# Performance work log

Measured on AMD Instinct MI355X. Metric: run time of the kernel, lower is better.

The kernel has to match this reference:

```python
import jax, jax.numpy as jnp
import numpy as np

EMBED_DIM = 1024
NUM_HEADS = 16
HEAD_DIM = EMBED_DIM // NUM_HEADS


def setup_inputs() -> dict:
    key = jax.random.key(0)
    ks = jax.random.split(key, 7)
    B, N, C = 2, 2048, EMBED_DIM
    s = 1.0 / np.sqrt(C)
    return {
        "x": jax.random.normal(ks[0], (B, N, C), dtype=jnp.float32),
        "phase_signal": jax.random.uniform(ks[1], (B,), dtype=jnp.float32),
        "qkv_w": jax.random.normal(ks[2], (3 * C, C), dtype=jnp.float32) * s,
        "qkv_b": jnp.zeros((3 * C,), dtype=jnp.float32),
        "proj_w": jax.random.normal(ks[3], (C, C), dtype=jnp.float32) * s,
        "proj_b": jnp.zeros((C,), dtype=jnp.float32),
        "phase_weight": jnp.ones((NUM_HEADS,), dtype=jnp.float32),
    }


def reference(x, phase_signal, qkv_w, qkv_b, proj_w, proj_b, phase_weight):
    B, N, C = x.shape
    H, D = NUM_HEADS, HEAD_DIM
    # qkv projection: [B,N,3C] -> [3,B,H,N,D]
    qkv = (x @ qkv_w.T + qkv_b).reshape(B, N, 3, H, D)
    qkv = jnp.transpose(qkv, (2, 0, 3, 1, 4))
    q, k, v = qkv[0], qkv[1], qkv[2]
    attn = jnp.einsum("bhnd,bhmd->bhnm", q, k) * (D ** -0.5)
    # per-(batch, head) phase modulation applied before softmax
    phase_mod = phase_weight[None, :, None, None] * phase_signal[:, None, None, None]
    attn = attn * (1.0 + 0.2 * phase_mod)
    attn = jax.nn.softmax(attn, axis=-1)  # dropout is identity in eval mode
    out = jnp.einsum("bhnm,bhmd->bhnd", attn, v)
    out = jnp.transpose(out, (0, 2, 1, 3)).reshape(B, N, C)
    return out @ proj_w.T + proj_b
```

## Files before the change

### kernel.cpp

```cpp
#include <hip/hip_runtime.h>
#include <stdint.h>

#define NUM_H 16
#define HD    64
#define CDIM  1024
#define NSEQ  2048
#define NBATCH 2
#define LOG2E 1.4426950408889634f

typedef __attribute__((ext_vector_type(8))) short short8;
typedef __attribute__((ext_vector_type(4))) float f32x4;
typedef __attribute__((ext_vector_type(16))) float f32x16;
typedef __attribute__((ext_vector_type(4))) unsigned short ushort4v;
typedef __attribute__((ext_vector_type(4))) float float4v;
typedef __attribute__((ext_vector_type(2))) unsigned int u32x2;

__device__ __forceinline__ unsigned short f2bf(float f) {
    unsigned int u = __builtin_bit_cast(unsigned int, f);
    unsigned int r = u + 0x7fffu + ((u >> 16) & 1u);
    return (unsigned short)(r >> 16);
}

__device__ __forceinline__ float bf2f(unsigned short u) {
    return __builtin_bit_cast(float, (unsigned int)u << 16);
}

__device__ __forceinline__ unsigned int cvtpk(float a, float b) {
    unsigned int r;
    asm("v_cvt_pk_bf16_f32 %0, %1, %2" : "=v"(r) : "v"(a), "v"(b));
    return r;
}

__device__ __forceinline__ void plswap(unsigned int &a, unsigned int &b) {
    asm("v_permlane32_swap_b32 %0, %1" : "+v"(a), "+v"(b));
}

__device__ __forceinline__ void gload_lds16(const void* g, const void* l) {
    __builtin_amdgcn_global_load_lds(
        (const __attribute__((address_space(1))) unsigned int*)(unsigned long long)(uintptr_t)g,
        (__attribute__((address_space(3))) unsigned int*)(unsigned int)(uintptr_t)l,
        16, 0, 0);
}

__global__ void cvt_all_kernel(const float* __restrict__ x,
                               const float* __restrict__ w1,
                               const float* __restrict__ wp,
                               unsigned short* __restrict__ xo,
                               unsigned short* __restrict__ w1o,
                               unsigned short* __restrict__ wpo) {
    int i = blockIdx.x * blockDim.x + threadIdx.x;
    const float* in; unsigned short* out;
    if (i < 1048576)      { in = x;  out = xo; }
    else if (i < 1835008) { in = w1; out = w1o; i -= 1048576; }
    else                  { in = wp; out = wpo; i -= 1835008; }
    float4v v = *(const float4v*)(in + (size_t)i * 4);
    ushort4v o;
    o[0] = f2bf(v[0]); o[1] = f2bf(v[1]); o[2] = f2bf(v[2]); o[3] = f2bf(v[3]);
    *(ushort4v*)(out + (size_t)i * 4) = o;
}

__global__ __launch_bounds__(512, 2) void gemm_qkv(
    const unsigned short* __restrict__ A,
    const unsigned short* __restrict__ Bw,
    const float* __restrict__ bias,
    const float* __restrict__ ps,
    const float* __restrict__ pw,
    unsigned short* __restrict__ qb,
    unsigned short* __restrict__ kfrag,
    unsigned short* __restrict__ vfrag)
{
    __shared__ unsigned short lds[2][2][2][128][64];

    const int tid = threadIdx.x;
    const int wid = tid >> 6;
    const int lane = tid & 63;
    const int l15 = lane & 15, l4 = lane >> 4;
    const int wave_m = wid >> 2, wave_n = wid & 3;

    const int bm = blockIdx.x;
    const int bn = blockIdx.y;

    f32x4 acc[8][4];
    const f32x4 zero4 = {0.f, 0.f, 0.f, 0.f};
#pragma unroll
    for (int m = 0; m < 8; ++m)
#pragma unroll
        for (int n = 0; n < 4; ++n) acc[m][n] = zero4;

    const int jr = lane >> 3;
    const int jc = ((lane & 7) ^ jr) << 4;
    const char* aB = (const char*)A  + (size_t)(bm * 256) * 2048;
    const char* bB = (const char*)Bw + (size_t)(bn * 256) * 2048;

    auto stageH = [&](int t, int which) {
        const int buf = t & 1;
        const int op = which >> 1, hf = which & 1;
        const char* src = (op == 0) ? aB : bB;
        const int rowb = hf * 128 + wid * 16;
        const size_t k0b = (size_t)t * 128;
        char* dst = (char*)&lds[buf][op][hf][wid * 16][0];
#pragma unroll
        for (int i = 0; i < 2; ++i)
            gload_lds16(src + (size_t)(rowb + i * 8 + jr) * 2048 + k0b + jc,
                        dst + i * 1024);
    };

    const int swz = (l15 & 7) << 4;
    auto rdA = [&](int buf, int mq, int mp, int kk) -> short8 {
        return *(const short8*)((const char*)&lds[buf][0][wave_m][mq * 64 + mp * 16 + l15][0]
                                + ((kk * 64 + l4 * 16) ^ swz));
    };
    auto rdB = [&](int buf, int nq, int np, int kk) -> short8 {
        const int br = wave_n * 64 + nq * 32 + np * 16 + l15;
        return *(const short8*)((const char*)&lds[buf][1][br >> 7][br & 127][0]
                                + ((kk * 64 + l4 * 16) ^ swz));
    };

    stageH(0, 0); stageH(0, 1); stageH(0, 2); stageH(0, 3);
    stageH(1, 2); stageH(1, 3); stageH(1, 0); stageH(1, 1);
    asm volatile("s_waitcnt vmcnt(8)" ::: "memory");
    __builtin_amdgcn_s_barrier();

    for (int t = 0; t < 16; ++t) {
        const int buf = t & 1;
        short8 af[4][2], bf[2][2][2];

#pragma unroll
        for (int mp = 0; mp < 4; ++mp) {
            af[mp][0] = rdA(buf, 0, mp, 0); af[mp][1] = rdA(buf, 0, mp, 1);
        }
#pragma unroll
        for (int np = 0; np < 2; ++np) {
            bf[0][np][0] = rdB(buf, 0, np, 0); bf[0][np][1] = rdB(buf, 0, np, 1);
        }
        __builtin_amdgcn_s_barrier();
        __builtin_amdgcn_s_setprio(1);
#pragma unroll
        for (int mp = 0; mp < 4; ++mp)
#pragma unroll
            for (int np = 0; np < 2; ++np)
#pragma unroll
                for (int kk = 0; kk < 2; ++kk)
                    acc[mp][np] = __builtin_amdgcn_mfma_f32_16x16x32_bf16(
                        af[mp][kk], bf[0][np][kk], acc[mp][np], 0, 0, 0);
        __builtin_amdgcn_s_setprio(0);
        __builtin_amdgcn_s_barrier();

#pragma unroll
        for (int np = 0; np < 2; ++np) {
            bf[1][np][0] = rdB(buf, 1, np, 0); bf[1][np][1] = rdB(buf, 1, np, 1);
        }
        if (t < 14) stageH(t + 2, 2);
        __builtin_amdgcn_s_barrier();
        __builtin_amdgcn_s_setprio(1);
#pragma unroll
        for (int mp = 0; mp < 4; ++mp)
#pragma unroll
            for (int np = 0; np < 2; ++np)
#pragma unroll
                for (int kk = 0; kk < 2; ++kk)
                    acc[mp][2 + np] = __builtin_amdgcn_mfma_f32_16x16x32_bf16(
                        af[mp][kk], bf[1][np][kk], acc[mp][2 + np], 0, 0, 0);
        __builtin_amdgcn_s_setprio(0);
        __builtin_amdgcn_s_barrier();

#pragma unroll
        for (int mp = 0; mp < 4; ++mp) {
            af[mp][0] = rdA(buf, 1, mp, 0); af[mp][1] = rdA(buf, 1, mp, 1);
        }
        if (t < 14) stageH(t + 2, 3);
        __builtin_amdgcn_s_barrier();
        __builtin_amdgcn_s_setprio(1);
#pragma unroll
        for (int mp = 0; mp < 4; ++mp)
#pragma unroll
            for (int np = 0; np < 2; ++np)
#pragma unroll
                for (int kk = 0; kk < 2; ++kk)
                    acc[4 + mp][np] = __builtin_amdgcn_mfma_f32_16x16x32_bf16(
                        af[mp][kk], bf[0][np][kk], acc[4 + mp][np], 0, 0, 0);
        __builtin_amdgcn_s_setprio(0);
        __builtin_amdgcn_s_barrier();

        if (t < 14) { stageH(t + 2, 0); stageH(t + 2, 1); }
        __builtin_amdgcn_s_barrier();
        __builtin_amdgcn_s_setprio(1);
#pragma unroll
        for (int mp = 0; mp < 4; ++mp)
#pragma unroll
            for (int np = 0; np < 2; ++np)
#pragma unroll
                for (int kk = 0; kk < 2; ++kk)
                    acc[4 + mp][2 + np] = __builtin_amdgcn_mfma_f32_16x16x32_bf16(
                        af[mp][kk], bf[1][np][kk], acc[4 + mp][2 + np], 0, 0, 0);
        __builtin_amdgcn_s_setprio(0);
        if (t < 14)       { asm volatile("s_waitcnt vmcnt(8)" ::: "memory"); }
        else if (t == 14) { asm volatile("s_waitcnt vmcnt(0)" ::: "memory"); }
        __builtin_amdgcn_s_barrier();
    }

    const int col_base = bn * 256 + wave_n * 64;
    const int t3b = bn >> 2;
    const int bb = bm >> 3;
    const int nn0 = (bm & 7) * 256;
    char* tbc = (char*)&lds[0][0][0][0][0];

    __syncthreads();

    if (t3b == 0) {
#pragma unroll
        for (int n = 0; n < 4; ++n) {
            const int d = n * 16 + l15;
            const float bv = bias[col_base + n * 16 + l15];
#pragma unroll
            for (int m = 0; m < 8; ++m) {
#pragma unroll
                for (int r = 0; r < 4; ++r) {
                    const int tt = wave_m * 128 + m * 16 + l4 * 4 + r;
                    *(unsigned short*)(tbc + wave_n * 32768 + tt * 128 +
                                       ((d * 2) ^ ((tt & 7) << 4))) = f2bf(acc[m][n][r] + bv);
                }
            }
        }
        __syncthreads();
#pragma unroll
        for (int i = 0; i < 16; ++i) {
            const int hq = i >> 2, sub = i & 3;
            const int tt = sub * 64 + (tid >> 3);
            const int chunk = tid & 7;
            const short8 v = *(const short8*)(tbc + hq * 32768 + tt * 128 +
                                              ((chunk * 16) ^ ((tt & 7) << 4)));
            *(short8*)(qb + ((size_t)(bb * 16 + bn * 4 + hq) * 2048 + nn0 + tt) * 64 + chunk * 8) = v;
        }
    } else if (t3b == 1) {
        const float ps0 = ps[0], ps1 = ps[1];
        const int hh = (bn - 4) * 4 + wave_n;
        const float kf = 0.125f * LOG2E *
                         (1.f + 0.2f * pw[hh] * ((bb == 0) ? ps0 : ps1));
#pragma unroll
        for (int n = 0; n < 4; ++n) {
            const int hi_ = l15 >> 3, e = l15 & 7;
            const float bv = bias[col_base + n * 16 + l15];
#pragma unroll
            for (int m = 0; m < 8; ++m) {
#pragma unroll
                for (int r = 0; r < 4; ++r) {
                    const int tt = wave_m * 128 + m * 16 + l4 * 4 + r;
                    const int ti = tt >> 6, u = tt & 63;
                    const int s_ = u >> 5, l31_ = u & 31;
                    *(unsigned short*)(tbc + (((wave_n * 4 + ti) * 8 + s_ * 4 + n) << 10) +
                                       ((hi_ * 32 + l31_) << 4) + e * 2) =
                        f2bf((acc[m][n][r] + bv) * kf);
                }
            }
        }
        __syncthreads();
#pragma unroll
        for (int i = 0; i < 16; ++i) {
            const int hq = i >> 2, ti = i & 3;
            const short8 v = *(const short8*)(tbc + i * 8192 + tid * 16);
            *(short8*)(kfrag + ((size_t)(bb * 16 + (bn - 4) * 4 + hq) * 32 +
                                ((bm & 7) * 4 + ti)) * 4096 + tid * 8) = v;
        }
    } else {
#pragma unroll
        for (int n = 0; n < 4; ++n) {
            const int d = n * 16 + l15;
            const int dt_ = n >> 1, l31_ = d & 31;
            const float bv = bias[col_base + n * 16 + l15];
#pragma unroll
            for (int m = 0; m < 8; ++m) {
#pragma unroll
                for (int r = 0; r < 4; ++r) {
                    const int tt = wave_m * 128 + m * 16 + l4 * 4 + r;
                    const int ti = tt >> 6, u = tt & 63;
                    const int ks = u >> 4, hi_ = (u >> 3) & 1, e = u & 7;
                    *(unsigned short*)(tbc + (((wave_n * 4 + ti) * 8 + dt_ * 4 + ks) << 10) +
                                       ((hi_ * 32 + l31_) << 4) + e * 2) =
                        f2bf(acc[m][n][r] + bv);
                }
            }
        }
        __syncthreads();
#pragma unroll
        for (int i = 0; i < 16; ++i) {
            const int hq = i >> 2, ti = i & 3;
            const short8 v = *(const short8*)(tbc + i * 8192 + tid * 16);
            *(short8*)(vfrag + ((size_t)(bb * 16 + (bn - 8) * 4 + hq) * 32 +
                                ((bm & 7) * 4 + ti)) * 4096 + tid * 8) = v;
        }
    }
}

__global__ __launch_bounds__(256, 2) void gemm_proj(
    const unsigned short* __restrict__ A,
    const unsigned short* __restrict__ Bw,
    const float* __restrict__ bias,
    float* __restrict__ out)
{
    __shared__ unsigned short As[2][128 * 64];
    __shared__ unsigned short Bs[2][128 * 64];
    const int tid = threadIdx.x;
    const int wid = tid >> 6;
    const int lane = tid & 63;
    const int l15 = lane & 15, l4 = lane >> 4;
    const int bm = blockIdx.x, bn = blockIdx.y;
    const int wr = wid >> 1, wc = wid & 1;

    f32x4 acc[4][4];
    const f32x4 zero4 = {0.f, 0.f, 0.f, 0.f};
#pragma unroll
    for (int m = 0; m < 4; ++m)
#pragma unroll
        for (int n = 0; n < 4; ++n) acc[m][n] = zero4;

    const int jr = lane >> 3;
    const int jc = ((lane & 7) ^ jr) << 4;
    const char* aB = (const char*)A  + (size_t)(bm * 128) * 2048;
    const char* bB = (const char*)Bw + (size_t)(bn * 128) * 2048;

    auto stage = [&](int buf, int k0) {
#pragma unroll
        for (int i = 0; i < 4; ++i) {
            const int rowb = wid * 32 + i * 8;
            gload_lds16(aB + (size_t)(rowb + jr) * 2048 + k0 * 2 + jc,
                        (const char*)&As[buf][0] + rowb * 128);
            gload_lds16(bB + (size_t)(rowb + jr) * 2048 + k0 * 2 + jc,
                        (const char*)&Bs[buf][0] + rowb * 128);
        }
    };

    const int swz = (l15 & 7) << 4;

    stage(0, 0);
    for (int it = 0; it < 16; ++it) {
        const int buf = it & 1;
        __syncthreads();
        if (it < 15) stage(buf ^ 1, (it + 1) * 64);
#pragma unroll
        for (int kk = 0; kk < 2; ++kk) {
            short8 a[4], b[4];
#pragma unroll
            for (int m = 0; m < 4; ++m)
                a[m] = *(const short8*)((const char*)&As[buf][0] +
                        (wr * 64 + m * 16 + l15) * 128 + ((kk * 64 + l4 * 16) ^ swz));
#pragma unroll
            for (int n = 0; n < 4; ++n)
                b[n] = *(const short8*)((const char*)&Bs[buf][0] +
                        (wc * 64 + n * 16 + l15) * 128 + ((kk * 64 + l4 * 16) ^ swz));
            __builtin_amdgcn_s_setprio(1);
#pragma unroll
            for (int m = 0; m < 4; ++m)
#pragma unroll
                for (int n = 0; n < 4; ++n)
                    acc[m][n] = __builtin_amdgcn_mfma_f32_16x16x32_bf16(a[m], b[n], acc[m][n], 0, 0, 0);
            __builtin_amdgcn_s_setprio(0);
        }
    }

    const int row_base = bm * 128 + wr * 64;
    const int col_base = bn * 128 + wc * 64;
#pragma unroll
    for (int n = 0; n < 4; ++n) {
        const int col = col_base + n * 16 + l15;
        const float bv = bias[col];
#pragma unroll
        for (int m = 0; m < 4; ++m) {
#pragma unroll
            for (int r = 0; r < 4; ++r) {
                const int row = row_base + m * 16 + l4 * 4 + r;
                out[(size_t)row * 1024 + col] = acc[m][n][r] + bv;
            }
        }
    }
}

__global__ __launch_bounds__(256, 4) void attn_kernel(
    const unsigned short* __restrict__ qb,
    const unsigned short* __restrict__ kfrag,
    const unsigned short* __restrict__ vfrag,
    unsigned short* __restrict__ o0,
    unsigned short* __restrict__ o1,
    float* __restrict__ lrb)
{
    __shared__ unsigned short KVs[2][2][4096];

    const int tid = threadIdx.x;
    const int w = tid >> 6;
    const int l = tid & 63;
    const int l31 = l & 31;
    const int hi = l >> 5;

    const int bid = blockIdx.y * 32 + blockIdx.x;
    const int wg = (bid & 7) * 128 + (bid >> 3);
    const int bh = wg >> 5;
    const int r5 = wg & 31;
    const int qt = r5 >> 1, kvh = r5 & 1;
    const int b = bh >> 4, h = bh & 15;
    const int q0 = qt * 128 + w * 32;

    const char* qg = (const char*)(qb + (size_t)bh * 2048 * 64);
    const unsigned short* kg = kfrag + ((size_t)bh * 32 + kvh * 16) * 4096;
    const unsigned short* vg = vfrag + ((size_t)bh * 32 + kvh * 16) * 4096;

    short8 qf[4];
#pragma unroll
    for (int t = 0; t < 4; ++t)
        qf[t] = *(const short8*)(qg + (size_t)(q0 + l31) * 128 + t * 32 + hi * 16);

    f32x16 oacc[2];
#pragma unroll
    for (int dt = 0; dt < 2; ++dt)
#pragma unroll
        for (int r = 0; r < 16; ++r) oacc[dt][r] = 0.f;
    float lr = 0.f;

    auto stage = [&](int buf, int T) {
#pragma unroll
        for (int i = 0; i < 2; ++i) {
            const int c = w * 2 + i;
            gload_lds16(kg + (size_t)T * 4096 + c * 512 + l * 8, &KVs[buf][0][c * 512]);
            gload_lds16(vg + (size_t)T * 4096 + c * 512 + l * 8, &KVs[buf][1][c * 512]);
        }
    };

    stage(0, 0);
    __syncthreads();

    for (int it = 0; it < 16; ++it) {
        const int buf = it & 1;
        if (it < 15) stage(buf ^ 1, it + 1);

        const unsigned short* Kb = &KVs[buf][0][0];
        const unsigned short* Vb = &KVs[buf][1][0];

        f32x16 sa[2];
        __builtin_amdgcn_s_setprio(1);
#pragma unroll
        for (int s = 0; s < 2; ++s) {
#pragma unroll
            for (int r = 0; r < 16; ++r) sa[s][r] = 0.f;
#pragma unroll
            for (int t = 0; t < 4; ++t) {
                const short8 kf = *(const short8*)(Kb + (s * 4 + t) * 512 + l * 8);
                sa[s] = __builtin_amdgcn_mfma_f32_32x32x16_bf16(kf, qf[t], sa[s], 0, 0, 0);
            }
        }
        __builtin_amdgcn_s_setprio(0);

#pragma unroll
        for (int s = 0; s < 2; ++s)
#pragma unroll
            for (int r = 0; r < 16; ++r)
                sa[s][r] = __builtin_amdgcn_exp2f(sa[s][r] - 20.0f);

        float ts[16];
#pragma unroll
        for (int r = 0; r < 16; ++r) ts[r] = sa[0][r] + sa[1][r];
#pragma unroll
        for (int d = 8; d >= 1; d >>= 1)
#pragma unroll
            for (int r = 0; r < 8; ++r)
                if (r < d) ts[r] += ts[r + d];
        lr += ts[0] + __shfl_xor(ts[0], 32);

#pragma unroll
        for (int s = 0; s < 2; ++s) {
            unsigned int wv[8];
#pragma unroll
            for (int g = 0; g < 8; ++g)
                wv[g] = cvtpk(sa[s][g * 2], sa[s][g * 2 + 1]);
            plswap(wv[0], wv[2]); plswap(wv[1], wv[3]);
            plswap(wv[4], wv[6]); plswap(wv[5], wv[7]);
            union { unsigned int u[4]; short8 s8; } f0, f1;
            f0.u[0] = wv[0]; f0.u[1] = wv[1]; f0.u[2] = wv[2]; f0.u[3] = wv[3];
            f1.u[0] = wv[4]; f1.u[1] = wv[5]; f1.u[2] = wv[6]; f1.u[3] = wv[7];
            __builtin_amdgcn_s_setprio(1);
#pragma unroll
            for (int dt = 0; dt < 2; ++dt) {
                const short8 v0 = *(const short8*)(Vb + (dt * 4 + s * 2 + 0) * 512 + l * 8);
                oacc[dt] = __builtin_amdgcn_mfma_f32_32x32x16_bf16(v0, f0.s8, oacc[dt], 0, 0, 0);
                const short8 v1 = *(const short8*)(Vb + (dt * 4 + s * 2 + 1) * 512 + l * 8);
                oacc[dt] = __builtin_amdgcn_mfma_f32_32x32x16_bf16(v1, f1.s8, oacc[dt], 0, 0, 0);
            }
            __builtin_amdgcn_s_setprio(0);
        }
        __syncthreads();
    }

    const float inv = 1.0f / lr;
    unsigned short* ob = kvh ? o1 : o0;
    char* outp = (char*)ob + ((size_t)(b * 2048 + q0 + l31) * 1024 + h * 64) * 2;
#pragma unroll
    for (int dt = 0; dt < 2; ++dt)
#pragma unroll
        for (int rg = 0; rg < 4; ++rg) {
            u32x2 pkd;
            pkd[0] = cvtpk(oacc[dt][rg * 4 + 0] * inv, oacc[dt][rg * 4 + 1] * inv);
            pkd[1] = cvtpk(oacc[dt][rg * 4 + 2] * inv, oacc[dt][rg * 4 + 3] * inv);
            *(u32x2*)(outp + (size_t)(dt * 32 + rg * 8 + hi * 4) * 2) = pkd;
        }
    if (hi == 0)
        lrb[(kvh << 16) + (bh << 11) + q0 + l31] = lr;
}

__global__ void combine_kernel(unsigned short* __restrict__ o0,
                               const unsigned short* __restrict__ o1,
                               const float* __restrict__ lrb) {
    const int idx = blockIdx.x * blockDim.x + threadIdx.x;
    const size_t e0 = (size_t)idx * 8;
    const int row = (int)(e0 >> 10);
    const int col = (int)(e0 & 1023);
    const int b = row >> 11, q = row & 2047, h = col >> 6;
    const int bhq = ((b * 16 + h) << 11) + q;
    const float l0 = lrb[bhq], l1 = lrb[65536 + bhq];
    const float w0 = l0 / (l0 + l1);
    const float w1 = 1.0f - w0;
    short8 v0 = *(short8*)(o0 + e0);
    const short8 v1 = *(const short8*)(o1 + e0);
    short8 o;
#pragma unroll
    for (int j = 0; j < 8; ++j)
        o[j] = (short)f2bf(bf2f((unsigned short)v0[j]) * w0 +
                           bf2f((unsigned short)v1[j]) * w1);
    *(short8*)(o0 + e0) = o;
}

extern "C" void kernel_launch(void* const* d_in, const int* in_sizes, int n_in,
                              void* d_out, int out_size, void* d_ws, size_t ws_size,
                              hipStream_t stream) {
    const float* x      = (const float*)d_in[0];
    const float* ps     = (const float*)d_in[1];
    const float* qkv_w  = (const float*)d_in[2];
    const float* qkv_b  = (const float*)d_in[3];
    const float* proj_w = (const float*)d_in[4];
    const float* proj_b = (const float*)d_in[5];
    const float* pw     = (const float*)d_in[6];
    float* out = (float*)d_out;
    char* ws = (char*)d_ws;

    unsigned short* x_bf    = (unsigned short*)(ws);
    unsigned short* w1_bf   = (unsigned short*)(ws + (8u  << 20));
    unsigned short* wp_bf   = (unsigned short*)(ws + (14u << 20));
    unsigned short* qb      = (unsigned short*)(ws + (16u << 20));
    unsigned short* kfrag   = (unsigned short*)(ws + (24u << 20));
    unsigned short* vfrag   = (unsigned short*)(ws + (32u << 20));
    unsigned short* o1      = (unsigned short*)(ws + (40u << 20));
    unsigned short* o0      = x_bf;
    float*          lrb     = (float*)w1_bf;
    unsigned short* attn_bf = o0;

    cvt_all_kernel<<<8192, 256, 0, stream>>>(x, qkv_w, proj_w, x_bf, w1_bf, wp_bf);
    gemm_qkv<<<dim3(16, 12), 512, 0, stream>>>(x_bf, w1_bf, qkv_b, ps, pw, qb, kfrag, vfrag);
    attn_kernel<<<dim3(32, 32), 256, 0, stream>>>(qb, kfrag, vfrag, o0, o1, lrb);
    combine_kernel<<<2048, 256, 0, stream>>>(o0, o1, lrb);
    gemm_proj<<<dim3(32, 8), 256, 0, stream>>>(attn_bf, wp_bf, proj_b, out);
}
```

Before: 113.0 us.

## Retile QKV GEMM to 256x192 with 12 waves; MFMA row-sums and deeper attention pipeline

The QKV GEMM moves from 256x256 tiles with 8 waves to 256x192 tiles with 12 waves, giving a 16x16 grid of blocks and a unified epilogue that handles Q/K/V per 64-column region. The attention kernel computes the softmax denominator with an MFMA against a ones vector instead of shuffle reductions. It also prefetches two K/V tiles ahead with explicit waitcnt-based synchronisation. These changes aim to improve CU occupancy and balance, remove ALU reduction work, and overlap loads better, at the cost of more LDS use and extra MFMA work.

```diff
diff --git a/kernel.cpp b/kernel.cpp
--- a/kernel.cpp
+++ b/kernel.cpp
@@ -59,7 +59,7 @@
     *(ushort4v*)(out + (size_t)i * 4) = o;
 }
 
-__global__ __launch_bounds__(512, 2) void gemm_qkv(
+__global__ __launch_bounds__(768, 3) void gemm_qkv(
     const unsigned short* __restrict__ A,
     const unsigned short* __restrict__ Bw,
     const float* __restrict__ bias,
@@ -69,225 +69,165 @@
     unsigned short* __restrict__ kfrag,
     unsigned short* __restrict__ vfrag)
 {
-    __shared__ unsigned short lds[2][2][2][128][64];
+    __shared__ unsigned short smem[57344];
+    unsigned short* As = smem;
+    unsigned short* Bs = smem + 32768;
 
     const int tid = threadIdx.x;
     const int wid = tid >> 6;
     const int lane = tid & 63;
     const int l15 = lane & 15, l4 = lane >> 4;
-    const int wave_m = wid >> 2, wave_n = wid & 3;
+    const int wave_n = wid >> 2;
+    const int wave_m = wid & 3;
 
     const int bm = blockIdx.x;
     const int bn = blockIdx.y;
 
-    f32x4 acc[8][4];
+    f32x4 acc[4][4];
     const f32x4 zero4 = {0.f, 0.f, 0.f, 0.f};
 #pragma unroll
-    for (int m = 0; m < 8; ++m)
+    for (int m = 0; m < 4; ++m)
 #pragma unroll
         for (int n = 0; n < 4; ++n) acc[m][n] = zero4;
 
     const int jr = lane >> 3;
     const int jc = ((lane & 7) ^ jr) << 4;
     const char* aB = (const char*)A  + (size_t)(bm * 256) * 2048;
-    const char* bB = (const char*)Bw + (size_t)(bn * 256) * 2048;
-
-    auto stageH = [&](int t, int which) {
+    const char* bB = (const char*)Bw + (size_t)(bn * 192) * 2048;
+
+    auto stage = [&](int t) {
         const int buf = t & 1;
-        const int op = which >> 1, hf = which & 1;
-        const char* src = (op == 0) ? aB : bB;
-        const int rowb = hf * 128 + wid * 16;
-        const size_t k0b = (size_t)t * 128;
-        char* dst = (char*)&lds[buf][op][hf][wid * 16][0];
-#pragma unroll
-        for (int i = 0; i < 2; ++i)
-            gload_lds16(src + (size_t)(rowb + i * 8 + jr) * 2048 + k0b + jc,
-                        dst + i * 1024);
+        const size_t kb = (size_t)t * 128;
+        for (int s = wid; s < 32; s += 12)
+            gload_lds16(aB + (size_t)(s * 8 + jr) * 2048 + kb + jc,
+                        (char*)(As + buf * 16384) + s * 1024);
+        for (int s = wid; s < 24; s += 12)
+            gload_lds16(bB + (size_t)(s * 8 + jr) * 2048 + kb + jc,
+                        (char*)(Bs + buf * 12288) + s * 1024);
     };
 
     const int swz = (l15 & 7) << 4;
-    auto rdA = [&](int buf, int mq, int mp, int kk) -> short8 {
-        return *(const short8*)((const char*)&lds[buf][0][wave_m][mq * 64 + mp * 16 + l15][0]
-                                + ((kk * 64 + l4 * 16) ^ swz));
-    };
-    auto rdB = [&](int buf, int nq, int np, int kk) -> short8 {
-        const int br = wave_n * 64 + nq * 32 + np * 16 + l15;
-        return *(const short8*)((const char*)&lds[buf][1][br >> 7][br & 127][0]
-                                + ((kk * 64 + l4 * 16) ^ swz));
-    };
-
-    stageH(0, 0); stageH(0, 1); stageH(0, 2); stageH(0, 3);
-    stageH(1, 2); stageH(1, 3); stageH(1, 0); stageH(1, 1);
-    asm volatile("s_waitcnt vmcnt(8)" ::: "memory");
+
+    stage(0); stage(1);
+    asm volatile("s_waitcnt vmcnt(4)" ::: "memory");
     __builtin_amdgcn_s_barrier();
 
     for (int t = 0; t < 16; ++t) {
         const int buf = t & 1;
-        short8 af[4][2], bf[2][2][2];
-
-#pragma unroll
-        for (int mp = 0; mp < 4; ++mp) {
-            af[mp][0] = rdA(buf, 0, mp, 0); af[mp][1] = rdA(buf, 0, mp, 1);
-        }
-#pragma unroll
-        for (int np = 0; np < 2; ++np) {
-            bf[0][np][0] = rdB(buf, 0, np, 0); bf[0][np][1] = rdB(buf, 0, np, 1);
-        }
+        __builtin_amdgcn_s_setprio(1);
+#pragma unroll
+        for (int kk = 0; kk < 2; ++kk) {
+            short8 a[4], b[4];
+#pragma unroll
+            for (int m = 0; m < 4; ++m)
+                a[m] = *(const short8*)((const char*)(As + buf * 16384) +
+                        (wave_m * 64 + m * 16 + l15) * 128 + ((kk * 64 + l4 * 16) ^ swz));
+#pragma unroll
+            for (int n = 0; n < 4; ++n)
+                b[n] = *(const short8*)((const char*)(Bs + buf * 12288) +
+                        (wave_n * 64 + n * 16 + l15) * 128 + ((kk * 64 + l4 * 16) ^ swz));
+#pragma unroll
+            for (int m = 0; m < 4; ++m)
+#pragma unroll
+                for (int n = 0; n < 4; ++n)
+                    acc[m][n] = __builtin_amdgcn_mfma_f32_16x16x32_bf16(a[m], b[n], acc[m][n], 0, 0, 0);
+        }
+        __builtin_amdgcn_s_setprio(0);
+        asm volatile("s_waitcnt lgkmcnt(0)" ::: "memory");
         __builtin_amdgcn_s_barrier();
-        __builtin_amdgcn_s_setprio(1);
-#pragma unroll
-        for (int mp = 0; mp < 4; ++mp)
-#pragma unroll
-            for (int np = 0; np < 2; ++np)
-#pragma unroll
-                for (int kk = 0; kk < 2; ++kk)
-                    acc[mp][np] = __builtin_amdgcn_mfma_f32_16x16x32_bf16(
-                        af[mp][kk], bf[0][np][kk], acc[mp][np], 0, 0, 0);
-        __builtin_amdgcn_s_setprio(0);
-        __builtin_amdgcn_s_barrier();
-
-#pragma unroll
-        for (int np = 0; np < 2; ++np) {
-            bf[1][np][0] = rdB(buf, 1, np, 0); bf[1][np][1] = rdB(buf, 1, np, 1);
-        }
-        if (t < 14) stageH(t + 2, 2);
-        __builtin_amdgcn_s_barrier();
-        __builtin_amdgcn_s_setprio(1);
-#pragma unroll
-        for (int mp = 0; mp < 4; ++mp)
-#pragma unroll
-            for (int np = 0; np < 2; ++np)
-#pragma unroll
-                for (int kk = 0; kk < 2; ++kk)
-                    acc[mp][2 + np] = __builtin_amdgcn_mfma_f32_16x16x32_bf16(
-                        af[mp][kk], bf[1][np][kk], acc[mp][2 + np], 0, 0, 0);
-        __builtin_amdgcn_s_setprio(0);
-        __builtin_amdgcn_s_barrier();
-
-#pragma unroll
-        for (int mp = 0; mp < 4; ++mp) {
-            af[mp][0] = rdA(buf, 1, mp, 0); af[mp][1] = rdA(buf, 1, mp, 1);
-        }
-        if (t < 14) stageH(t + 2, 3);
-        __builtin_amdgcn_s_barrier();
-        __builtin_amdgcn_s_setprio(1);
-#pragma unroll
-        for (int mp = 0; mp < 4; ++mp)
-#pragma unroll
-            for (int np = 0; np < 2; ++np)
-#pragma unroll
-                for (int kk = 0; kk < 2; ++kk)
-                    acc[4 + mp][np] = __builtin_amdgcn_mfma_f32_16x16x32_bf16(
-                        af[mp][kk], bf[0][np][kk], acc[4 + mp][np], 0, 0, 0);
-        __builtin_amdgcn_s_setprio(0);
-        __builtin_amdgcn_s_barrier();
-
-        if (t < 14) { stageH(t + 2, 0); stageH(t + 2, 1); }
-        __builtin_amdgcn_s_barrier();
-        __builtin_amdgcn_s_setprio(1);
-#pragma unroll
-        for (int mp = 0; mp < 4; ++mp)
-#pragma unroll
-            for (int np = 0; np < 2; ++np)
-#pragma unroll
-                for (int kk = 0; kk < 2; ++kk)
-                    acc[4 + mp][2 + np] = __builtin_amdgcn_mfma_f32_16x16x32_bf16(
-                        af[mp][kk], bf[1][np][kk], acc[4 + mp][2 + np], 0, 0, 0);
-        __builtin_amdgcn_s_setprio(0);
-        if (t < 14)       { asm volatile("s_waitcnt vmcnt(8)" ::: "memory"); }
-        else if (t == 14) { asm volatile("s_waitcnt vmcnt(0)" ::: "memory"); }
+        if (t < 14) {
+            stage(t + 2);
+            asm volatile("s_waitcnt vmcnt(4)" ::: "memory");
+        } else if (t == 14) {
+            asm volatile("s_waitcnt vmcnt(0)" ::: "memory");
+        }
         __builtin_amdgcn_s_barrier();
     }
 
-    const int col_base = bn * 256 + wave_n * 64;
-    const int t3b = bn >> 2;
+    __syncthreads();
+    char* tbc = (char*)smem;
     const int bb = bm >> 3;
-    const int nn0 = (bm & 7) * 256;
-    char* tbc = (char*)&lds[0][0][0][0][0];
-
-    __syncthreads();
-
-    if (t3b == 0) {
+    const int cb = bn * 192 + wave_n * 64;
+    const int t3w = cb >> 10;
+    const int hh_w = (cb >> 6) & 15;
+    float kf = 1.f;
+    if (t3w == 1)
+        kf = 0.125f * LOG2E * (1.f + 0.2f * pw[hh_w] * ((bb == 0) ? ps[0] : ps[1]));
+
+    if (t3w == 0) {
 #pragma unroll
         for (int n = 0; n < 4; ++n) {
             const int d = n * 16 + l15;
-            const float bv = bias[col_base + n * 16 + l15];
-#pragma unroll
-            for (int m = 0; m < 8; ++m) {
+            const float bv = bias[cb + n * 16 + l15];
+#pragma unroll
+            for (int m = 0; m < 4; ++m)
 #pragma unroll
                 for (int r = 0; r < 4; ++r) {
-                    const int tt = wave_m * 128 + m * 16 + l4 * 4 + r;
+                    const int tt = wave_m * 64 + m * 16 + l4 * 4 + r;
                     *(unsigned short*)(tbc + wave_n * 32768 + tt * 128 +
                                        ((d * 2) ^ ((tt & 7) << 4))) = f2bf(acc[m][n][r] + bv);
                 }
-            }
-        }
-        __syncthreads();
-#pragma unroll
-        for (int i = 0; i < 16; ++i) {
-            const int hq = i >> 2, sub = i & 3;
-            const int tt = sub * 64 + (tid >> 3);
-            const int chunk = tid & 7;
-            const short8 v = *(const short8*)(tbc + hq * 32768 + tt * 128 +
-                                              ((chunk * 16) ^ ((tt & 7) << 4)));
-            *(short8*)(qb + ((size_t)(bb * 16 + bn * 4 + hq) * 2048 + nn0 + tt) * 64 + chunk * 8) = v;
-        }
-    } else if (t3b == 1) {
-        const float ps0 = ps[0], ps1 = ps[1];
-        const int hh = (bn - 4) * 4 + wave_n;
-        const float kf = 0.125f * LOG2E *
-                         (1.f + 0.2f * pw[hh] * ((bb == 0) ? ps0 : ps1));
+        }
+    } else if (t3w == 1) {
 #pragma unroll
         for (int n = 0; n < 4; ++n) {
             const int hi_ = l15 >> 3, e = l15 & 7;
-            const float bv = bias[col_base + n * 16 + l15];
-#pragma unroll
-            for (int m = 0; m < 8; ++m) {
+            const float bv = bias[cb + n * 16 + l15];
+#pragma unroll
+            for (int m = 0; m < 4; ++m)
 #pragma unroll
                 for (int r = 0; r < 4; ++r) {
-                    const int tt = wave_m * 128 + m * 16 + l4 * 4 + r;
-                    const int ti = tt >> 6, u = tt & 63;
+                    const int tt = wave_m * 64 + m * 16 + l4 * 4 + r;
+                    const int T_ = tt >> 6, u = tt & 63;
                     const int s_ = u >> 5, l31_ = u & 31;
-                    *(unsigned short*)(tbc + (((wave_n * 4 + ti) * 8 + s_ * 4 + n) << 10) +
+                    *(unsigned short*)(tbc + wave_n * 32768 + ((T_ * 8 + s_ * 4 + n) << 10) +
                                        ((hi_ * 32 + l31_) << 4) + e * 2) =
                         f2bf((acc[m][n][r] + bv) * kf);
                 }
-            }
-        }
-        __syncthreads();
-#pragma unroll
-        for (int i = 0; i < 16; ++i) {
-            const int hq = i >> 2, ti = i & 3;
-            const short8 v = *(const short8*)(tbc + i * 8192 + tid * 16);
-            *(short8*)(kfrag + ((size_t)(bb * 16 + (bn - 4) * 4 + hq) * 32 +
-                                ((bm & 7) * 4 + ti)) * 4096 + tid * 8) = v;
         }
     } else {
 #pragma unroll
         for (int n = 0; n < 4; ++n) {
-            const int d = n * 16 + l15;
-            const int dt_ = n >> 1, l31_ = d & 31;
-            const float bv = bias[col_base + n * 16 + l15];
-#pragma unroll
-            for (int m = 0; m < 8; ++m) {
+            const int dt_ = n >> 1;
+            const int l31v = (n & 1) * 16 + l15;
+            const float bv = bias[cb + n * 16 + l15];
+#pragma unroll
+            for (int m = 0; m < 4; ++m)
 #pragma unroll
                 for (int r = 0; r < 4; ++r) {
-                    const int tt = wave_m * 128 + m * 16 + l4 * 4 + r;
-                    const int ti = tt >> 6, u = tt & 63;
+                    const int tt = wave_m * 64 + m * 16 + l4 * 4 + r;
+                    const int T_ = tt >> 6, u = tt & 63;
                     const int ks = u >> 4, hi_ = (u >> 3) & 1, e = u & 7;
-                    *(unsigned short*)(tbc + (((wave_n * 4 + ti) * 8 + dt_ * 4 + ks) << 10) +
-                                       ((hi_ * 32 + l31_) << 4) + e * 2) =
+                    *(unsigned short*)(tbc + wave_n * 32768 + ((T_ * 8 + dt_ * 4 + ks) << 10) +
+                                       ((hi_ * 32 + l31v) << 4) + e * 2) =
                         f2bf(acc[m][n][r] + bv);
                 }
-            }
-        }
-        __syncthreads();
-#pragma unroll
-        for (int i = 0; i < 16; ++i) {
-            const int hq = i >> 2, ti = i & 3;
-            const short8 v = *(const short8*)(tbc + i * 8192 + tid * 16);
-            *(short8*)(vfrag + ((size_t)(bb * 16 + (bn - 8) * 4 + hq) * 32 +
-                                ((bm & 7) * 4 + ti)) * 4096 + tid * 8) = v;
+        }
+    }
+    __syncthreads();
+
+#pragma unroll
+    for (int i = 0; i < 8; ++i) {
+        const int flat = (i * 768 + tid) * 16;
+        const int region = flat >> 15;
+        const int cbr = bn * 192 + region * 64;
+        const int t3r = cbr >> 10;
+        const int hhr = (cbr >> 6) & 15;
+        const int within = flat & 32767;
+        if (t3r == 0) {
+            const int tt = within >> 7;
+            const int chunk = (within >> 4) & 7;
+            const short8 v = *(const short8*)(tbc + region * 32768 + tt * 128 +
+                                              ((chunk * 16) ^ ((tt & 7) << 4)));
+            *(short8*)(qb + ((size_t)(bb * 16 + hhr) * 2048 + (bm & 7) * 256 + tt) * 64 +
+                       chunk * 8) = v;
+        } else {
+            const int c2 = within >> 13;
+            const int off = within & 8191;
+            const short8 v = *(const short8*)(tbc + region * 32768 + c2 * 8192 + off);
+            unsigned short* dstb = (t3r == 1) ? kfrag : vfrag;
+            *(short8*)(dstb + ((size_t)(bb * 16 + hhr) * 32 + (bm & 7) * 4 + c2) * 4096 +
+                       (off >> 1)) = v;
         }
     }
 }
@@ -408,12 +348,13 @@
     for (int t = 0; t < 4; ++t)
         qf[t] = *(const short8*)(qg + (size_t)(q0 + l31) * 128 + t * 32 + hi * 16);
 
-    f32x16 oacc[2];
-#pragma unroll
-    for (int dt = 0; dt < 2; ++dt)
-#pragma unroll
-        for (int r = 0; r < 16; ++r) oacc[dt][r] = 0.f;
-    float lr = 0.f;
+    short8 ones;
+#pragma unroll
+    for (int j = 0; j < 8; ++j) ones[j] = (short)0x3F80;
+
+    f32x16 oacc[2], lacc;
+#pragma unroll
+    for (int r = 0; r < 16; ++r) { oacc[0][r] = 0.f; oacc[1][r] = 0.f; lacc[r] = 0.f; }
 
     auto stage = [&](int buf, int T) {
 #pragma unroll
@@ -424,13 +365,12 @@
         }
     };
 
-    stage(0, 0);
-    __syncthreads();
+    stage(0, 0); stage(1, 1);
+    asm volatile("s_waitcnt vmcnt(4)" ::: "memory");
+    __builtin_amdgcn_s_barrier();
 
     for (int it = 0; it < 16; ++it) {
         const int buf = it & 1;
-        if (it < 15) stage(buf ^ 1, it + 1);
-
         const unsigned short* Kb = &KVs[buf][0][0];
         const unsigned short* Vb = &KVs[buf][1][0];
 
@@ -453,16 +393,6 @@
 #pragma unroll
             for (int r = 0; r < 16; ++r)
                 sa[s][r] = __builtin_amdgcn_exp2f(sa[s][r] - 20.0f);
-
-        float ts[16];
-#pragma unroll
-        for (int r = 0; r < 16; ++r) ts[r] = sa[0][r] + sa[1][r];
-#pragma unroll
-        for (int d = 8; d >= 1; d >>= 1)
-#pragma unroll
-            for (int r = 0; r < 8; ++r)
-                if (r < d) ts[r] += ts[r + d];
-        lr += ts[0] + __shfl_xor(ts[0], 32);
 
 #pragma unroll
         for (int s = 0; s < 2; ++s) {
@@ -476,6 +406,8 @@
             f0.u[0] = wv[0]; f0.u[1] = wv[1]; f0.u[2] = wv[2]; f0.u[3] = wv[3];
             f1.u[0] = wv[4]; f1.u[1] = wv[5]; f1.u[2] = wv[6]; f1.u[3] = wv[7];
             __builtin_amdgcn_s_setprio(1);
+            lacc = __builtin_amdgcn_mfma_f32_32x32x16_bf16(ones, f0.s8, lacc, 0, 0, 0);
+            lacc = __builtin_amdgcn_mfma_f32_32x32x16_bf16(ones, f1.s8, lacc, 0, 0, 0);
 #pragma unroll
             for (int dt = 0; dt < 2; ++dt) {
                 const short8 v0 = *(const short8*)(Vb + (dt * 4 + s * 2 + 0) * 512 + l * 8);
@@ -485,10 +417,21 @@
             }
             __builtin_amdgcn_s_setprio(0);
         }
-        __syncthreads();
+
+        if (it < 15) {
+            asm volatile("s_waitcnt lgkmcnt(0)" ::: "memory");
+            __builtin_amdgcn_s_barrier();
+            if (it < 14) {
+                stage(buf, it + 2);
+                asm volatile("s_waitcnt vmcnt(4)" ::: "memory");
+            } else {
+                asm volatile("s_waitcnt vmcnt(0)" ::: "memory");
+            }
+            __builtin_amdgcn_s_barrier();
+        }
     }
 
-    const float inv = 1.0f / lr;
+    const float inv = 1.0f / lacc[0];
     unsigned short* ob = kvh ? o1 : o0;
     char* outp = (char*)ob + ((size_t)(b * 2048 + q0 + l31) * 1024 + h * 64) * 2;
 #pragma unroll
@@ -501,7 +444,7 @@
             *(u32x2*)(outp + (size_t)(dt * 32 + rg * 8 + hi * 4) * 2) = pkd;
         }
     if (hi == 0)
-        lrb[(kvh << 16) + (bh << 11) + q0 + l31] = lr;
+        lrb[(kvh << 16) + (bh << 11) + q0 + l31] = lacc[0];
 }
 
 __global__ void combine_kernel(unsigned short* __restrict__ o0,
@@ -548,11 +491,10 @@
     unsigned short* o1      = (unsigned short*)(ws + (40u << 20));
     unsigned short* o0      = x_bf;
     float*          lrb     = (float*)w1_bf;
-    unsigned short* attn_bf = o0;
 
     cvt_all_kernel<<<8192, 256, 0, stream>>>(x, qkv_w, proj_w, x_bf, w1_bf, wp_bf);
-    gemm_qkv<<<dim3(16, 12), 512, 0, stream>>>(x_bf, w1_bf, qkv_b, ps, pw, qb, kfrag, vfrag);
+    gemm_qkv<<<dim3(16, 16), 768, 0, stream>>>(x_bf, w1_bf, qkv_b, ps, pw, qb, kfrag, vfrag);
     attn_kernel<<<dim3(32, 32), 256, 0, stream>>>(qb, kfrag, vfrag, o0, o1, lrb);
     combine_kernel<<<2048, 256, 0, stream>>>(o0, o1, lrb);
-    gemm_proj<<<dim3(32, 8), 256, 0, stream>>>(attn_bf, wp_bf, proj_b, out);
-}
+    gemm_proj<<<dim3(32, 8), 256, 0, stream>>>(o0, wp_bf, proj_b, out);
+}
```

Result: no change. 112.6 us (-0.3%).
